# Performance work log

Hardware: AMD Instinct MI355X
Metric: run time of the kernel (lower is better)

The kernel has to match this reference:

```python
import jax, jax.numpy as jnp
import numpy as np

TOP_K = 2


def setup_inputs() -> dict:
    key = jax.random.key(0)
    kx, kw = jax.random.split(key)
    x = jax.random.normal(kx, (4, 4096, 2048), dtype=jnp.float32)
    router_weights = jax.random.normal(kw, (8, 2048), dtype=jnp.float32) * 0.02
    return {"x": x, "router_weights": router_weights}


def reference(x, router_weights):
    # logits[b,s,e] = sum_d x[b,s,d] * W[e,d]
    logits = jnp.einsum('bsd,ed->bse', x, router_weights)
    # top-k over experts, then softmax over the selected k logits
    top_vals, top_idx = jax.lax.top_k(logits, TOP_K)  # [B,S,K]
    gates = jax.nn.softmax(top_vals, axis=-1)
    indices = top_idx.astype(jnp.int32)
    return indices, gates, logits
```

## Files before the change

kernel.cpp:

```cpp
#include <hip/hip_runtime.h>
#include <math.h>


constexpr int D      = 2048;
constexpr int E      = 8;
constexpr int T      = 8;
constexpr int WAVES  = 4;
constexpr int TOKENS = 16384;

__device__ __forceinline__ bool better(float va, int ia, float vb, int ib) {
    return (va > vb) || (va == vb && ia < ib);
}

__global__ __launch_bounds__(256, 2)
void moe_router_kernel(const float* __restrict__ x,
                       const float* __restrict__ w,
                       float* __restrict__ out)
{
    __shared__ float scr[WAVES][64][64];

    const int lane = threadIdx.x & 63;
    const int wave = threadIdx.x >> 6;
    const int tok0 = (blockIdx.x * WAVES + wave) * T;

    float acc[T * E];
#pragma unroll
    for (int i = 0; i < T * E; ++i) acc[i] = 0.0f;

#pragma unroll
    for (int it = 0; it < D / 256; ++it) {
        const int d = it * 256 + lane * 4;
        float4 wv[E];
#pragma unroll
        for (int e = 0; e < E; ++e)
            wv[e] = *reinterpret_cast<const float4*>(w + e * D + d);
        float4 xv[T];
#pragma unroll
        for (int t = 0; t < T; ++t)
            xv[t] = *reinterpret_cast<const float4*>(x + (size_t)(tok0 + t) * D + d);
#pragma unroll
        for (int t = 0; t < T; ++t) {
#pragma unroll
            for (int e = 0; e < E; ++e) {
                float a = acc[t * E + e];
                a = fmaf(xv[t].x, wv[e].x, a);
                a = fmaf(xv[t].y, wv[e].y, a);
                a = fmaf(xv[t].z, wv[e].z, a);
                a = fmaf(xv[t].w, wv[e].w, a);
                acc[t * E + e] = a;
            }
        }
    }

#pragma unroll
    for (int p = 0; p < 64; ++p)
        scr[wave][p][(lane + p) & 63] = acc[p];

    __syncthreads();

    float s0 = 0.f, s1 = 0.f, s2 = 0.f, s3 = 0.f;
#pragma unroll
    for (int j = 0; j < 64; j += 4) {
        s0 += scr[wave][lane][(lane + j + 0) & 63];
        s1 += scr[wave][lane][(lane + j + 1) & 63];
        s2 += scr[wave][lane][(lane + j + 2) & 63];
        s3 += scr[wave][lane][(lane + j + 3) & 63];
    }
    const float logit = (s0 + s1) + (s2 + s3);

    const int t     = lane >> 3;
    const int e     = lane & 7;
    const int token = tok0 + t;

    float* out_idx    = out;
    float* out_gate   = out + TOKENS * 2;
    float* out_logits = out + TOKENS * 4;

    out_logits[(size_t)token * E + e] = logit;

    float v1 = logit, v2 = -INFINITY;
    int   i1 = e,     i2 = E;
#pragma unroll
    for (int m = 1; m <= 4; m <<= 1) {
        float ov1 = __shfl_xor(v1, m, 64);
        int   oi1 = __shfl_xor(i1, m, 64);
        float ov2 = __shfl_xor(v2, m, 64);
        int   oi2 = __shfl_xor(i2, m, 64);
        float nv1, nv2; int ni1, ni2;
        if (better(v1, i1, ov1, oi1)) {
            nv1 = v1; ni1 = i1;
            if (better(v2, i2, ov1, oi1)) { nv2 = v2;  ni2 = i2;  }
            else                          { nv2 = ov1; ni2 = oi1; }
        } else {
            nv1 = ov1; ni1 = oi1;
            if (better(ov2, oi2, v1, i1)) { nv2 = ov2; ni2 = oi2; }
            else                          { nv2 = v1;  ni2 = i1;  }
        }
        v1 = nv1; i1 = ni1; v2 = nv2; i2 = ni2;
    }

    if (e < 2) {
        const float ed  = expf(v2 - v1);
        const float inv = 1.0f / (1.0f + ed);
        const float g   = (e == 0) ? inv : ed * inv;
        out_idx [token * 2 + e] = (float)((e == 0) ? i1 : i2);
        out_gate[token * 2 + e] = g;
    }
}

extern "C" void kernel_launch(void* const* d_in, const int* in_sizes, int n_in,
                              void* d_out, int out_size, void* d_ws, size_t ws_size,
                              hipStream_t stream) {
    const float* x = (const float*)d_in[0];
    const float* w = (const float*)d_in[1];
    float* out = (float*)d_out;
    hipLaunchKernelGGL(moe_router_kernel, dim3(512), dim3(256), 0, stream,
                       x, w, out);
}
```

Measured before the change: 190.1 us.

## Split each wave into 4 tokens × 16 lanes and reduce via shuffles

Work is remapped so each wave handles 4 tokens, with 16 lanes per token striding across D, replacing the 8-tokens-per-wave, 64-lane layout. The LDS transpose-reduction and __syncthreads are replaced by a butterfly shuffle reduce-scatter that leaves one logit per lane. x loads are nontemporal, the register footprint drops from 64 accumulators to 8, launch bounds request 4 blocks per SIMD, and the grid doubles. The aim is more occupancy and memory parallelism for this bandwidth-bound read of x. The cost is that W is reused across fewer tokens per load, so W traffic from cache rises.

```diff
diff --git a/kernel.cpp b/kernel.cpp
--- a/kernel.cpp
+++ b/kernel.cpp
@@ -4,79 +4,87 @@
 
 constexpr int D      = 2048;
 constexpr int E      = 8;
-constexpr int T      = 8;
-constexpr int WAVES  = 4;
+constexpr int T_W    = 4;
+constexpr int LPT    = 16;
+constexpr int ITERS  = D / (LPT * 4);
 constexpr int TOKENS = 16384;
+
+typedef float f32x4 __attribute__((ext_vector_type(4)));
 
 __device__ __forceinline__ bool better(float va, int ia, float vb, int ib) {
     return (va > vb) || (va == vb && ia < ib);
 }
 
-__global__ __launch_bounds__(256, 2)
+__global__ __launch_bounds__(256, 4)
 void moe_router_kernel(const float* __restrict__ x,
                        const float* __restrict__ w,
                        float* __restrict__ out)
 {
-    __shared__ float scr[WAVES][64][64];
-
     const int lane = threadIdx.x & 63;
     const int wave = threadIdx.x >> 6;
-    const int tok0 = (blockIdx.x * WAVES + wave) * T;
+    const int tloc = lane >> 4;
+    const int g    = lane & 15;
+    const int token = (blockIdx.x * 4 + wave) * T_W + tloc;
 
-    float acc[T * E];
+    const float* xp = x + (size_t)token * D + g * 4;
+    const float* wp = w + g * 4;
+
+    float acc[E];
 #pragma unroll
-    for (int i = 0; i < T * E; ++i) acc[i] = 0.0f;
+    for (int e = 0; e < E; ++e) acc[e] = 0.0f;
 
+#pragma unroll 4
+    for (int it = 0; it < ITERS; ++it) {
+        const f32x4 xv = __builtin_nontemporal_load(
+            reinterpret_cast<const f32x4*>(xp + it * (LPT * 4)));
 #pragma unroll
-    for (int it = 0; it < D / 256; ++it) {
-        const int d = it * 256 + lane * 4;
-        float4 wv[E];
-#pragma unroll
-        for (int e = 0; e < E; ++e)
-            wv[e] = *reinterpret_cast<const float4*>(w + e * D + d);
-        float4 xv[T];
-#pragma unroll
-        for (int t = 0; t < T; ++t)
-            xv[t] = *reinterpret_cast<const float4*>(x + (size_t)(tok0 + t) * D + d);
-#pragma unroll
-        for (int t = 0; t < T; ++t) {
-#pragma unroll
-            for (int e = 0; e < E; ++e) {
-                float a = acc[t * E + e];
-                a = fmaf(xv[t].x, wv[e].x, a);
-                a = fmaf(xv[t].y, wv[e].y, a);
-                a = fmaf(xv[t].z, wv[e].z, a);
-                a = fmaf(xv[t].w, wv[e].w, a);
-                acc[t * E + e] = a;
-            }
+        for (int e = 0; e < E; ++e) {
+            const f32x4 wv =
+                *reinterpret_cast<const f32x4*>(wp + e * D + it * (LPT * 4));
+            float a = acc[e];
+            a = fmaf(xv.x, wv.x, a);
+            a = fmaf(xv.y, wv.y, a);
+            a = fmaf(xv.z, wv.z, a);
+            a = fmaf(xv.w, wv.w, a);
+            acc[e] = a;
         }
     }
 
 #pragma unroll
-    for (int p = 0; p < 64; ++p)
-        scr[wave][p][(lane + p) & 63] = acc[p];
+    for (int e = 0; e < E; ++e) acc[e] += __shfl_xor(acc[e], 8, 64);
 
-    __syncthreads();
+    const bool s4 = (lane & 4) != 0;
+    float r[4];
+#pragma unroll
+    for (int i = 0; i < 4; ++i) {
+        const float keep = s4 ? acc[i + 4] : acc[i];
+        const float send = s4 ? acc[i]     : acc[i + 4];
+        r[i] = keep + __shfl_xor(send, 4, 64);
+    }
+    const bool s2 = (lane & 2) != 0;
+    float sr[2];
+#pragma unroll
+    for (int i = 0; i < 2; ++i) {
+        const float keep = s2 ? r[i + 2] : r[i];
+        const float send = s2 ? r[i]     : r[i + 2];
+        sr[i] = keep + __shfl_xor(send, 2, 64);
+    }
+    const bool s1 = (lane & 1) != 0;
+    float logit;
+    {
+        const float keep = s1 ? sr[1] : sr[0];
+        const float send = s1 ? sr[0] : sr[1];
+        logit = keep + __shfl_xor(send, 1, 64);
+    }
 
-    float s0 = 0.f, s1 = 0.f, s2 = 0.f, s3 = 0.f;
-#pragma unroll
-    for (int j = 0; j < 64; j += 4) {
-        s0 += scr[wave][lane][(lane + j + 0) & 63];
-        s1 += scr[wave][lane][(lane + j + 1) & 63];
-        s2 += scr[wave][lane][(lane + j + 2) & 63];
-        s3 += scr[wave][lane][(lane + j + 3) & 63];
-    }
-    const float logit = (s0 + s1) + (s2 + s3);
-
-    const int t     = lane >> 3;
-    const int e     = lane & 7;
-    const int token = tok0 + t;
+    const int  e      = lane & 7;
+    const bool writer = (lane & 8) == 0;
 
     float* out_idx    = out;
     float* out_gate   = out + TOKENS * 2;
     float* out_logits = out + TOKENS * 4;
 
-    out_logits[(size_t)token * E + e] = logit;
+    if (writer) out_logits[(size_t)token * E + e] = logit;
 
     float v1 = logit, v2 = -INFINITY;
     int   i1 = e,     i2 = E;
@@ -99,12 +107,12 @@
         v1 = nv1; i1 = ni1; v2 = nv2; i2 = ni2;
     }
 
-    if (e < 2) {
+    if (writer && e < 2) {
         const float ed  = expf(v2 - v1);
         const float inv = 1.0f / (1.0f + ed);
-        const float g   = (e == 0) ? inv : ed * inv;
+        const float gte = (e == 0) ? inv : ed * inv;
         out_idx [token * 2 + e] = (float)((e == 0) ? i1 : i2);
-        out_gate[token * 2 + e] = g;
+        out_gate[token * 2 + e] = gte;
     }
 }
 
@@ -114,6 +122,6 @@
     const float* x = (const float*)d_in[0];
     const float* w = (const float*)d_in[1];
     float* out = (float*)d_out;
-    hipLaunchKernelGGL(moe_router_kernel, dim3(512), dim3(256), 0, stream,
+    hipLaunchKernelGGL(moe_router_kernel, dim3(1024), dim3(256), 0, stream,
                        x, w, out);
 }
```

New measurement: 209.6 us. +10.3%, slower.

## Halve tokens per wave and replace LDS transpose with shuffle butterfly reduction

Applied to the files above, without the earlier changes.

Each wave now handles 4 tokens instead of 8 and the grid doubles, so each thread keeps 32 accumulators and the kernel can target 4 blocks per CU. The shared-memory transpose and __syncthreads used for the cross-lane reduction are replaced by a recursive-halving butterfly of xor shuffles that leaves one logit per lane. Weight loads are moved inside the expert loop and the D loop is only partially unrolled, which lowers register pressure. The cost is that the weight matrix is read by twice as many waves, and each wave issues fewer independent loads in flight.

```diff
diff --git a/kernel.cpp b/kernel.cpp
--- a/kernel.cpp
+++ b/kernel.cpp
@@ -4,21 +4,21 @@
 
 constexpr int D      = 2048;
 constexpr int E      = 8;
-constexpr int T      = 8;
+constexpr int T      = 4;
 constexpr int WAVES  = 4;
 constexpr int TOKENS = 16384;
+
+typedef float f32x4 __attribute__((ext_vector_type(4)));
 
 __device__ __forceinline__ bool better(float va, int ia, float vb, int ib) {
     return (va > vb) || (va == vb && ia < ib);
 }
 
-__global__ __launch_bounds__(256, 2)
+__global__ __launch_bounds__(256, 4)
 void moe_router_kernel(const float* __restrict__ x,
                        const float* __restrict__ w,
                        float* __restrict__ out)
 {
-    __shared__ float scr[WAVES][64][64];
-
     const int lane = threadIdx.x & 63;
     const int wave = threadIdx.x >> 6;
     const int tok0 = (blockIdx.x * WAVES + wave) * T;
@@ -27,56 +27,81 @@
 #pragma unroll
     for (int i = 0; i < T * E; ++i) acc[i] = 0.0f;
 
-#pragma unroll
+#pragma unroll 4
     for (int it = 0; it < D / 256; ++it) {
         const int d = it * 256 + lane * 4;
-        float4 wv[E];
-#pragma unroll
-        for (int e = 0; e < E; ++e)
-            wv[e] = *reinterpret_cast<const float4*>(w + e * D + d);
-        float4 xv[T];
+        f32x4 xv[T];
 #pragma unroll
         for (int t = 0; t < T; ++t)
-            xv[t] = *reinterpret_cast<const float4*>(x + (size_t)(tok0 + t) * D + d);
+            xv[t] = *reinterpret_cast<const f32x4*>(x + (size_t)(tok0 + t) * D + d);
 #pragma unroll
-        for (int t = 0; t < T; ++t) {
+        for (int e = 0; e < E; ++e) {
+            const f32x4 wv = *reinterpret_cast<const f32x4*>(w + e * D + d);
 #pragma unroll
-            for (int e = 0; e < E; ++e) {
+            for (int t = 0; t < T; ++t) {
                 float a = acc[t * E + e];
-                a = fmaf(xv[t].x, wv[e].x, a);
-                a = fmaf(xv[t].y, wv[e].y, a);
-                a = fmaf(xv[t].z, wv[e].z, a);
-                a = fmaf(xv[t].w, wv[e].w, a);
+                a = fmaf(xv[t].x, wv.x, a);
+                a = fmaf(xv[t].y, wv.y, a);
+                a = fmaf(xv[t].z, wv.z, a);
+                a = fmaf(xv[t].w, wv.w, a);
                 acc[t * E + e] = a;
             }
         }
     }
 
 #pragma unroll
-    for (int p = 0; p < 64; ++p)
-        scr[wave][p][(lane + p) & 63] = acc[p];
+    for (int i = 0; i < 32; ++i) acc[i] += __shfl_xor(acc[i], 32, 64);
 
-    __syncthreads();
+    const bool s16 = (lane & 16) != 0;
+    float r16[16];
+#pragma unroll
+    for (int i = 0; i < 16; ++i) {
+        const float keep = s16 ? acc[i + 16] : acc[i];
+        const float send = s16 ? acc[i]      : acc[i + 16];
+        r16[i] = keep + __shfl_xor(send, 16, 64);
+    }
+    const bool s8 = (lane & 8) != 0;
+    float r8[8];
+#pragma unroll
+    for (int i = 0; i < 8; ++i) {
+        const float keep = s8 ? r16[i + 8] : r16[i];
+        const float send = s8 ? r16[i]     : r16[i + 8];
+        r8[i] = keep + __shfl_xor(send, 8, 64);
+    }
+    const bool s4 = (lane & 4) != 0;
+    float r4[4];
+#pragma unroll
+    for (int i = 0; i < 4; ++i) {
+        const float keep = s4 ? r8[i + 4] : r8[i];
+        const float send = s4 ? r8[i]     : r8[i + 4];
+        r4[i] = keep + __shfl_xor(send, 4, 64);
+    }
+    const bool s2 = (lane & 2) != 0;
+    float r2[2];
+#pragma unroll
+    for (int i = 0; i < 2; ++i) {
+        const float keep = s2 ? r4[i + 2] : r4[i];
+        const float send = s2 ? r4[i]     : r4[i + 2];
+        r2[i] = keep + __shfl_xor(send, 2, 64);
+    }
+    const bool s1 = (lane & 1) != 0;
+    float logit;
+    {
+        const float keep = s1 ? r2[1] : r2[0];
+        const float send = s1 ? r2[0] : r2[1];
+        logit = keep + __shfl_xor(send, 1, 64);
+    }
 
-    float s0 = 0.f, s1 = 0.f, s2 = 0.f, s3 = 0.f;
-#pragma unroll
-    for (int j = 0; j < 64; j += 4) {
-        s0 += scr[wave][lane][(lane + j + 0) & 63];
-        s1 += scr[wave][lane][(lane + j + 1) & 63];
-        s2 += scr[wave][lane][(lane + j + 2) & 63];
-        s3 += scr[wave][lane][(lane + j + 3) & 63];
-    }
-    const float logit = (s0 + s1) + (s2 + s3);
-
-    const int t     = lane >> 3;
-    const int e     = lane & 7;
-    const int token = tok0 + t;
+    const int  e      = lane & 7;
+    const int  t      = (lane >> 3) & 3;
+    const int  token  = tok0 + t;
+    const bool writer = lane < 32;
 
     float* out_idx    = out;
     float* out_gate   = out + TOKENS * 2;
     float* out_logits = out + TOKENS * 4;
 
-    out_logits[(size_t)token * E + e] = logit;
+    if (writer) out_logits[(size_t)tok0 * E + lane] = logit;
 
     float v1 = logit, v2 = -INFINITY;
     int   i1 = e,     i2 = E;
@@ -99,7 +124,7 @@
         v1 = nv1; i1 = ni1; v2 = nv2; i2 = ni2;
     }
 
-    if (e < 2) {
+    if (writer && e < 2) {
         const float ed  = expf(v2 - v1);
         const float inv = 1.0f / (1.0f + ed);
         const float g   = (e == 0) ? inv : ed * inv;
@@ -114,6 +139,6 @@
     const float* x = (const float*)d_in[0];
     const float* w = (const float*)d_in[1];
     float* out = (float*)d_out;
-    hipLaunchKernelGGL(moe_router_kernel, dim3(512), dim3(256), 0, stream,
+    hipLaunchKernelGGL(moe_router_kernel, dim3(1024), dim3(256), 0, stream,
                        x, w, out);
 }
```

Measured after the change: 194.7 us. 1.02x slower.
